# Performance work log

Hardware: AMD Instinct MI355X
Metric: run time of the kernel (lower is better)

Reference implementation:

```python
import jax, jax.numpy as jnp
import numpy as np

N_EXPERTS = 8
D_MODEL = 1024
D_FFN = 4096
BATCH, SEQ = 4, 1024


def setup_inputs() -> dict:
    key = jax.random.key(0)
    ks = jax.random.split(key, 12)
    T = BATCH * SEQ
    s_d = 1.0 / np.sqrt(D_MODEL)
    s_f = 1.0 / np.sqrt(D_FFN)
    return {
        "x": jax.random.normal(ks[0], (BATCH, SEQ, D_MODEL), jnp.float32),
        "noise": jax.random.normal(ks[1], (T, N_EXPERTS), jnp.float32),
        # router (torch Linear stored as [out,in]; we store pre-transposed [in,out])
        "Wg": jax.random.uniform(ks[2], (D_MODEL, N_EXPERTS), jnp.float32, -s_d, s_d),
        "bg": jax.random.uniform(ks[3], (N_EXPERTS,), jnp.float32, -s_d, s_d),
        "Wn": jax.random.uniform(ks[4], (D_MODEL, N_EXPERTS), jnp.float32, -s_d, s_d),
        "bn": jax.random.uniform(ks[5], (N_EXPERTS,), jnp.float32, -s_d, s_d),
        # stacked expert weights: fc1 [E, D, F], fc2 [E, F, D]
        "W1": jax.random.uniform(ks[6], (N_EXPERTS, D_MODEL, D_FFN), jnp.float32, -s_d, s_d),
        "b1": jax.random.uniform(ks[7], (N_EXPERTS, D_FFN), jnp.float32, -s_d, s_d),
        "W2": jax.random.uniform(ks[8], (N_EXPERTS, D_FFN, D_MODEL), jnp.float32, -s_f, s_f),
        "b2": jax.random.uniform(ks[9], (N_EXPERTS, D_MODEL), jnp.float32, -s_f, s_f),
        "top_k": 2,
    }


def reference(x, noise, Wg, bg, Wn, bn, W1, b1, W2, b2, top_k):
    B, S, D = x.shape
    xf = x.reshape(-1, D)                       # [T, D]
    T = xf.shape[0]
    # --- noisy top-k router ---
    logits = xf @ Wg + bg                       # [T, E]
    noise_logits = xf @ Wn + bn                 # [T, E]
    noisy = logits + noise * jax.nn.softplus(noise_logits)
    top_v, top_i = jax.lax.top_k(noisy, top_k)  # [T, k]
    sparse = jnp.full_like(noisy, -jnp.inf)
    sparse = sparse.at[jnp.arange(T)[:, None], top_i].set(top_v)
    gates = jax.nn.softmax(sparse, axis=-1)     # [T, E], zeros off top-k
    # --- experts (dense grouped GEMM; non-selected tokens zeroed by gates) ---
    h = jax.nn.relu(jnp.einsum('td,edf->etf', xf, W1) + b1[:, None, :])  # [E, T, F]
    eo = jnp.einsum('etf,efd->etd', h, W2) + b2[:, None, :]              # [E, T, D]
    out = jnp.einsum('etd,te->td', eo, gates)                            # [T, D]
    return out.reshape(B, S, D)
```

## Files before the change

kernel.cpp:

```cpp
#include <hip/hip_runtime.h>
#include <math.h>

#define T_TOK 4096
#define DM 1024
#define DF 4096
#define NE 8

#define BM 128
#define BN 128
#define BK 64

typedef __attribute__((ext_vector_type(8))) short bf16x8;
typedef __attribute__((ext_vector_type(4))) float f32x4;
typedef unsigned long long u64;

__device__ __forceinline__ unsigned short f2bf(float f) {
    union { float f; unsigned int u; } v; v.f = f;
    unsigned int r = v.u + 0x7FFFu + ((v.u >> 16) & 1u);
    return (unsigned short)(r >> 16);
}
__device__ __forceinline__ float bf2f(unsigned short u) {
    union { float f; unsigned int u; } v; v.u = ((unsigned int)u) << 16;
    return v.f;
}
__device__ __forceinline__ u64 pk4(float4 a) {
    return (u64)f2bf(a.x) | ((u64)f2bf(a.y) << 16) | ((u64)f2bf(a.z) << 32) | ((u64)f2bf(a.w) << 48);
}

__device__ __forceinline__ void glds16(const void* g, void* l) {
    __builtin_amdgcn_global_load_lds(
        (const __attribute__((address_space(1))) unsigned int*)g,
        (__attribute__((address_space(3))) unsigned int*)l, 16, 0, 0);
}

__global__ __launch_bounds__(256) void k_router(
    const float* __restrict__ x, const float* __restrict__ noise,
    const float* __restrict__ Wg, const float* __restrict__ bg,
    const float* __restrict__ Wn, const float* __restrict__ bn,
    int* __restrict__ counts, int* __restrict__ slots, float* __restrict__ gates,
    unsigned short* __restrict__ xb)
{
    const int lane = threadIdx.x & 63;
    const int wave = threadIdx.x >> 6;
    const int t = blockIdx.x * 4 + wave;
    const float* xr = x + (size_t)t * DM;

    float4 xv[4];
    #pragma unroll
    for (int j = 0; j < 4; ++j) xv[j] = *(const float4*)(xr + j * 256 + lane * 4);
    #pragma unroll
    for (int j = 0; j < 4; ++j)
        *(u64*)(xb + (size_t)t * DM + j * 256 + lane * 4) = pk4(xv[j]);

    float accg[8], accn[8];
    #pragma unroll
    for (int i = 0; i < 8; ++i) { accg[i] = 0.f; accn[i] = 0.f; }

    #pragma unroll
    for (int j = 0; j < 4; ++j) {
        const float xs[4] = {xv[j].x, xv[j].y, xv[j].z, xv[j].w};
        #pragma unroll
        for (int jj = 0; jj < 4; ++jj) {
            int d = j * 256 + lane * 4 + jj;
            float xvv = xs[jj];
            float4 g0 = *(const float4*)(Wg + d * 8);
            float4 g1 = *(const float4*)(Wg + d * 8 + 4);
            float4 n0 = *(const float4*)(Wn + d * 8);
            float4 n1 = *(const float4*)(Wn + d * 8 + 4);
            accg[0] += xvv * g0.x; accg[1] += xvv * g0.y; accg[2] += xvv * g0.z; accg[3] += xvv * g0.w;
            accg[4] += xvv * g1.x; accg[5] += xvv * g1.y; accg[6] += xvv * g1.z; accg[7] += xvv * g1.w;
            accn[0] += xvv * n0.x; accn[1] += xvv * n0.y; accn[2] += xvv * n0.z; accn[3] += xvv * n0.w;
            accn[4] += xvv * n1.x; accn[5] += xvv * n1.y; accn[6] += xvv * n1.z; accn[7] += xvv * n1.w;
        }
    }
    #pragma unroll
    for (int s = 1; s < 64; s <<= 1) {
        #pragma unroll
        for (int e = 0; e < 8; ++e) {
            accg[e] += __shfl_xor(accg[e], s, 64);
            accn[e] += __shfl_xor(accn[e], s, 64);
        }
    }
    if (lane == 0) {
        float nv[8];
        #pragma unroll
        for (int e = 0; e < 8; ++e) {
            float lg = accg[e] + bg[e];
            float nl = accn[e] + bn[e];
            float sp = (nl > 20.f) ? nl : log1pf(expf(nl));
            nv[e] = lg + noise[(size_t)t * NE + e] * sp;
        }
        int i0 = 0;
        #pragma unroll
        for (int e = 1; e < 8; ++e) if (nv[e] > nv[i0]) i0 = e;
        int i1 = -1;
        #pragma unroll
        for (int e = 0; e < 8; ++e) {
            if (e == i0) continue;
            if (i1 < 0 || nv[e] > nv[i1]) i1 = e;
        }
        float ex = expf(nv[i1] - nv[i0]);
        float g0 = 1.f / (1.f + ex);
        float g1 = ex / (1.f + ex);
        int p0 = atomicAdd(counts + i0, 1);
        slots[i0 * T_TOK + p0] = t * 2;     gates[i0 * T_TOK + p0] = g0;
        int p1 = atomicAdd(counts + i1, 1);
        slots[i1 * T_TOK + p1] = t * 2 + 1; gates[i1 * T_TOK + p1] = g1;
    }
}

__global__ __launch_bounds__(256) void k_tr(const float* __restrict__ in,
                                            unsigned short* __restrict__ out,
                                            int R, int C)
{
    __shared__ unsigned short t[64 * 68];
    const int e = blockIdx.z;
    const int C0 = blockIdx.x * 64, R0 = blockIdx.y * 64;
    const float* ip = in + ((size_t)e * R + R0) * C + C0;
    unsigned short* op = out + ((size_t)e * C + C0) * R + R0;
    const int tid = threadIdx.x;

    #pragma unroll
    for (int p = 0; p < 4; ++p) {
        int r = p * 16 + (tid >> 4), c4 = (tid & 15) * 4;
        float4 v = *(const float4*)(ip + (size_t)r * C + c4);
        t[(c4 + 0) * 68 + r] = f2bf(v.x);
        t[(c4 + 1) * 68 + r] = f2bf(v.y);
        t[(c4 + 2) * 68 + r] = f2bf(v.z);
        t[(c4 + 3) * 68 + r] = f2bf(v.w);
    }
    __syncthreads();
    #pragma unroll
    for (int p = 0; p < 4; ++p) {
        int c = p * 16 + (tid >> 4), r4 = (tid & 15) * 4;
        u64 v = *(const u64*)(t + c * 68 + r4);
        *(u64*)(op + (size_t)c * R + r4) = v;
    }
}

__global__ __launch_bounds__(256, 4) void k_fc1(
    const unsigned short* __restrict__ xb, const unsigned short* __restrict__ W1t,
    const float* __restrict__ b1, const int* __restrict__ counts,
    const int* __restrict__ slots, unsigned short* __restrict__ h)
{
    const int e = blockIdx.x;
    const int cnt = counts[e];
    const int mt = blockIdx.z;
    if (mt * BM >= cnt) return;
    const int nb = blockIdx.y * BN;

    int offE = 0;
    for (int i = 0; i < e; ++i) offE += counts[i];

    __shared__ unsigned short As[BM * BK];
    __shared__ unsigned short Bs[BN * BK];
    __shared__ int slot_s[BM];

    const int tid = threadIdx.x;
    if (tid < BM) {
        int gi = mt * BM + tid;
        slot_s[tid] = (gi < cnt) ? slots[e * T_TOK + gi] : -1;
    }
    __syncthreads();

    const int lane = tid & 63, wv = tid >> 6;
    const int srow = tid >> 3;
    const int g = (tid & 7) ^ (srow & 7);

    const unsigned short* agp[4];
    const unsigned short* bgp[4];
    const unsigned short* wbase = W1t + (size_t)e * DF * DM;
    #pragma unroll
    for (int cc = 0; cc < 4; ++cc) {
        int row = cc * 32 + srow;
        int s = slot_s[row];
        int tok = (s >= 0) ? (s >> 1) : 0;
        agp[cc] = xb + (size_t)tok * DM + g * 8;
        bgp[cc] = wbase + (size_t)(nb + row) * DM + g * 8;
    }
    unsigned short* al = As + wv * 512;
    unsigned short* bl = Bs + wv * 512;

    const int wm = (wv & 1) * 64, wn = (wv >> 1) * 64;
    const int ml = lane & 15, kg = lane >> 4;

    f32x4 acc[4][4];
    #pragma unroll
    for (int ni = 0; ni < 4; ++ni)
        #pragma unroll
        for (int mi = 0; mi < 4; ++mi) acc[ni][mi] = (f32x4){0.f, 0.f, 0.f, 0.f};

    for (int k0 = 0; k0 < DM; k0 += BK) {
        #pragma unroll
        for (int cc = 0; cc < 4; ++cc) glds16(agp[cc] + k0, al + cc * 2048);
        #pragma unroll
        for (int cc = 0; cc < 4; ++cc) glds16(bgp[cc] + k0, bl + cc * 2048);
        __syncthreads();
        #pragma unroll
        for (int ks = 0; ks < 2; ++ks) {
            const int rch = (((ks * 4 + kg) ^ (ml & 7)) << 3);
            bf16x8 af[4], bfr[4];
            #pragma unroll
            for (int mi = 0; mi < 4; ++mi)
                af[mi] = *(const bf16x8*)(As + (wm + mi * 16 + ml) * BK + rch);
            #pragma unroll
            for (int ni = 0; ni < 4; ++ni)
                bfr[ni] = *(const bf16x8*)(Bs + (wn + ni * 16 + ml) * BK + rch);
            #pragma unroll
            for (int ni = 0; ni < 4; ++ni)
                #pragma unroll
                for (int mi = 0; mi < 4; ++mi)
                    acc[ni][mi] = __builtin_amdgcn_mfma_f32_16x16x32_bf16(bfr[ni], af[mi], acc[ni][mi], 0, 0, 0);
        }
        __syncthreads();
    }

    #pragma unroll
    for (int mi = 0; mi < 4; ++mi) {
        int row = wm + mi * 16 + ml;
        int s = slot_s[row];
        if (s < 0) continue;
        unsigned short* hrow = h + (size_t)(offE + mt * BM + row) * DF + nb;
        #pragma unroll
        for (int ni = 0; ni < 4; ++ni) {
            int n0 = wn + ni * 16 + kg * 4;
            float4 bb = *(const float4*)(b1 + (size_t)e * DF + nb + n0);
            float v0 = fmaxf(acc[ni][mi][0] + bb.x, 0.f);
            float v1 = fmaxf(acc[ni][mi][1] + bb.y, 0.f);
            float v2 = fmaxf(acc[ni][mi][2] + bb.z, 0.f);
            float v3 = fmaxf(acc[ni][mi][3] + bb.w, 0.f);
            u64 p = (u64)f2bf(v0) | ((u64)f2bf(v1) << 16) | ((u64)f2bf(v2) << 32) | ((u64)f2bf(v3) << 48);
            *(u64*)(hrow + n0) = p;
        }
    }
}

__global__ __launch_bounds__(256, 4) void k_fc2(
    const unsigned short* __restrict__ h, const unsigned short* __restrict__ W2t,
    const float* __restrict__ b2, const int* __restrict__ counts,
    const int* __restrict__ slots, const float* __restrict__ gates,
    unsigned short* __restrict__ eo)
{
    const int e = blockIdx.x;
    const int cnt = counts[e];
    const int mt = blockIdx.z >> 1;
    const int kz = blockIdx.z & 1;
    if (mt * BM >= cnt) return;
    const int nb = blockIdx.y * BN;

    int offE = 0;
    for (int i = 0; i < e; ++i) offE += counts[i];

    __shared__ unsigned short As[BM * BK];
    __shared__ unsigned short Bs[BN * BK];
    __shared__ int slot_s[BM];
    __shared__ float gate_s[BM];

    const int tid = threadIdx.x;
    if (tid < BM) {
        int gi = mt * BM + tid;
        if (gi < cnt) {
            slot_s[tid] = slots[e * T_TOK + gi];
            gate_s[tid] = gates[e * T_TOK + gi];
        } else { slot_s[tid] = -1; gate_s[tid] = 0.f; }
    }
    __syncthreads();

    const int lane = tid & 63, wv = tid >> 6;
    const int srow = tid >> 3;
    const int g = (tid & 7) ^ (srow & 7);
    const int kbeg = kz * (DF / 2);

    const unsigned short* agp[4];
    const unsigned short* bgp[4];
    const unsigned short* wbase = W2t + (size_t)e * DM * DF;
    #pragma unroll
    for (int cc = 0; cc < 4; ++cc) {
        int row = cc * 32 + srow;
        int gi = mt * BM + row;
        int gpos = offE + ((gi < cnt) ? gi : 0);
        agp[cc] = h + (size_t)gpos * DF + kbeg + g * 8;
        bgp[cc] = wbase + (size_t)(nb + row) * DF + kbeg + g * 8;
    }
    unsigned short* al = As + wv * 512;
    unsigned short* bl = Bs + wv * 512;

    const int wm = (wv & 1) * 64, wn = (wv >> 1) * 64;
    const int ml = lane & 15, kg = lane >> 4;

    f32x4 acc[4][4];
    #pragma unroll
    for (int ni = 0; ni < 4; ++ni)
        #pragma unroll
        for (int mi = 0; mi < 4; ++mi) acc[ni][mi] = (f32x4){0.f, 0.f, 0.f, 0.f};

    for (int k0 = 0; k0 < DF / 2; k0 += BK) {
        #pragma unroll
        for (int cc = 0; cc < 4; ++cc) glds16(agp[cc] + k0, al + cc * 2048);
        #pragma unroll
        for (int cc = 0; cc < 4; ++cc) glds16(bgp[cc] + k0, bl + cc * 2048);
        __syncthreads();
        #pragma unroll
        for (int ks = 0; ks < 2; ++ks) {
            const int rch = (((ks * 4 + kg) ^ (ml & 7)) << 3);
            bf16x8 af[4], bfr[4];
            #pragma unroll
            for (int mi = 0; mi < 4; ++mi)
                af[mi] = *(const bf16x8*)(As + (wm + mi * 16 + ml) * BK + rch);
            #pragma unroll
            for (int ni = 0; ni < 4; ++ni)
                bfr[ni] = *(const bf16x8*)(Bs + (wn + ni * 16 + ml) * BK + rch);
            #pragma unroll
            for (int ni = 0; ni < 4; ++ni)
                #pragma unroll
                for (int mi = 0; mi < 4; ++mi)
                    acc[ni][mi] = __builtin_amdgcn_mfma_f32_16x16x32_bf16(bfr[ni], af[mi], acc[ni][mi], 0, 0, 0);
        }
        __syncthreads();
    }

    unsigned short* eob = eo + (size_t)kz * 2 * T_TOK * DM;
    #pragma unroll
    for (int mi = 0; mi < 4; ++mi) {
        int row = wm + mi * 16 + ml;
        int s = slot_s[row];
        if (s < 0) continue;
        float gg = gate_s[row];
        #pragma unroll
        for (int ni = 0; ni < 4; ++ni) {
            int n0 = wn + ni * 16 + kg * 4;
            float4 bb;
            if (kz == 0) bb = *(const float4*)(b2 + (size_t)e * DM + nb + n0);
            else         bb = make_float4(0.f, 0.f, 0.f, 0.f);
            float v0 = gg * (acc[ni][mi][0] + bb.x);
            float v1 = gg * (acc[ni][mi][1] + bb.y);
            float v2 = gg * (acc[ni][mi][2] + bb.z);
            float v3 = gg * (acc[ni][mi][3] + bb.w);
            u64 p = (u64)f2bf(v0) | ((u64)f2bf(v1) << 16) | ((u64)f2bf(v2) << 32) | ((u64)f2bf(v3) << 48);
            *(u64*)(eob + (size_t)s * DM + nb + n0) = p;
        }
    }
}

__global__ __launch_bounds__(256) void k_comb(const unsigned short* __restrict__ eo,
                                              float* __restrict__ out)
{
    int i = blockIdx.x * 256 + threadIdx.x;
    int t = i >> 8;
    int d4 = (i & 255) * 4;
    const unsigned short* p0 = eo + (size_t)(2 * t) * DM + d4;
    const unsigned short* p1 = p0 + DM;
    const unsigned short* q0 = p0 + (size_t)2 * T_TOK * DM;
    const unsigned short* q1 = q0 + DM;
    ushort4 a0 = *(const ushort4*)p0;
    ushort4 a1 = *(const ushort4*)p1;
    ushort4 b0 = *(const ushort4*)q0;
    ushort4 b1 = *(const ushort4*)q1;
    float4 r;
    r.x = bf2f(a0.x) + bf2f(a1.x) + bf2f(b0.x) + bf2f(b1.x);
    r.y = bf2f(a0.y) + bf2f(a1.y) + bf2f(b0.y) + bf2f(b1.y);
    r.z = bf2f(a0.z) + bf2f(a1.z) + bf2f(b0.z) + bf2f(b1.z);
    r.w = bf2f(a0.w) + bf2f(a1.w) + bf2f(b0.w) + bf2f(b1.w);
    ((float4*)out)[i] = r;
}

extern "C" void kernel_launch(void* const* d_in, const int* in_sizes, int n_in,
                              void* d_out, int out_size, void* d_ws, size_t ws_size,
                              hipStream_t stream) {
    const float* x     = (const float*)d_in[0];
    const float* noise = (const float*)d_in[1];
    const float* Wg    = (const float*)d_in[2];
    const float* bg    = (const float*)d_in[3];
    const float* Wn    = (const float*)d_in[4];
    const float* bn    = (const float*)d_in[5];
    const float* W1    = (const float*)d_in[6];
    const float* b1    = (const float*)d_in[7];
    const float* W2    = (const float*)d_in[8];
    const float* b2    = (const float*)d_in[9];
    float* out = (float*)d_out;

    char* ws = (char*)d_ws;
    int*   counts = (int*)ws;
    int*   slots  = (int*)(ws + 4096);
    float* gates  = (float*)(ws + 4096 + NE * T_TOK * 4);
    unsigned short* xb = (unsigned short*)(ws + 4096 + 2 * NE * T_TOK * 4);
    unsigned short* hh = xb + (size_t)T_TOK * DM;
    unsigned short* Wt = hh + (size_t)2 * T_TOK * DF;
    unsigned short* eo = Wt + (size_t)NE * DM * DF;

    hipMemsetAsync(counts, 0, 4096, stream);

    k_router<<<T_TOK / 4, 256, 0, stream>>>(x, noise, Wg, bg, Wn, bn, counts, slots, gates, xb);

    k_tr<<<dim3(DF / 64, DM / 64, NE), 256, 0, stream>>>(W1, Wt, DM, DF);
    k_fc1<<<dim3(NE, DF / BN, T_TOK / BM), 256, 0, stream>>>(xb, Wt, b1, counts, slots, hh);

    k_tr<<<dim3(DM / 64, DF / 64, NE), 256, 0, stream>>>(W2, Wt, DF, DM);
    k_fc2<<<dim3(NE, DM / BN, (T_TOK / BM) * 2), 256, 0, stream>>>(hh, Wt, b2, counts, slots, gates, eo);

    k_comb<<<T_TOK * DM / 1024, 256, 0, stream>>>(eo, out);
}
```

Measured before the change: 760.3 us.

## Switch expert GEMMs to 32x32 MFMA with double-buffered LDS and wider split-K

New measurement: 824.1 us. 1.08x slower.

```diff
diff --git a/kernel.cpp b/kernel.cpp
--- a/kernel.cpp
+++ b/kernel.cpp
@@ -8,10 +8,10 @@
 
 #define BM 128
 #define BN 128
-#define BK 64
+#define BK 32
 
 typedef __attribute__((ext_vector_type(8))) short bf16x8;
-typedef __attribute__((ext_vector_type(4))) float f32x4;
+typedef __attribute__((ext_vector_type(16))) float f32x16;
 typedef unsigned long long u64;
 
 __device__ __forceinline__ unsigned short f2bf(float f) {
@@ -138,7 +138,7 @@
     }
 }
 
-__global__ __launch_bounds__(256, 4) void k_fc1(
+__global__ __launch_bounds__(256, 5) void k_fc1(
     const unsigned short* __restrict__ xb, const unsigned short* __restrict__ W1t,
     const float* __restrict__ b1, const int* __restrict__ counts,
     const int* __restrict__ slots, unsigned short* __restrict__ h)
@@ -152,215 +152,209 @@
     int offE = 0;
     for (int i = 0; i < e; ++i) offE += counts[i];
 
-    __shared__ unsigned short As[BM * BK];
-    __shared__ unsigned short Bs[BN * BK];
-    __shared__ int slot_s[BM];
+    __shared__ unsigned short As[2][4096];
+    __shared__ unsigned short Bs[2][4096];
 
     const int tid = threadIdx.x;
-    if (tid < BM) {
-        int gi = mt * BM + tid;
-        slot_s[tid] = (gi < cnt) ? slots[e * T_TOK + gi] : -1;
-    }
-    __syncthreads();
-
     const int lane = tid & 63, wv = tid >> 6;
-    const int srow = tid >> 3;
-    const int g = (tid & 7) ^ (srow & 7);
-
-    const unsigned short* agp[4];
-    const unsigned short* bgp[4];
-    const unsigned short* wbase = W1t + (size_t)e * DF * DM;
-    #pragma unroll
-    for (int cc = 0; cc < 4; ++cc) {
-        int row = cc * 32 + srow;
-        int s = slot_s[row];
-        int tok = (s >= 0) ? (s >> 1) : 0;
-        agp[cc] = xb + (size_t)tok * DM + g * 8;
-        bgp[cc] = wbase + (size_t)(nb + row) * DM + g * 8;
-    }
-    unsigned short* al = As + wv * 512;
-    unsigned short* bl = Bs + wv * 512;
+
+    const int srow = tid & 127;
+    const int pl0 = tid >> 7;
+    int sgi = mt * BM + srow;
+    int sA = (sgi < cnt) ? slots[e * T_TOK + sgi] : -1;
+    int tok = (sA >= 0) ? (sA >> 1) : 0;
+    const unsigned short* aptr = xb + (size_t)tok * DM + pl0 * 8;
+    const unsigned short* bptr = W1t + (size_t)e * DF * DM + (size_t)(nb + srow) * DM + pl0 * 8;
+    unsigned short* alds = &As[0][tid * 8];
+    unsigned short* blds = &Bs[0][tid * 8];
 
     const int wm = (wv & 1) * 64, wn = (wv >> 1) * 64;
-    const int ml = lane & 15, kg = lane >> 4;
-
-    f32x4 acc[4][4];
-    #pragma unroll
-    for (int ni = 0; ni < 4; ++ni)
-        #pragma unroll
-        for (int mi = 0; mi < 4; ++mi) acc[ni][mi] = (f32x4){0.f, 0.f, 0.f, 0.f};
-
+    const int l31 = lane & 31, lh = lane >> 5;
+
+    f32x16 acc[2][2];
+    #pragma unroll
+    for (int ni = 0; ni < 2; ++ni)
+        #pragma unroll
+        for (int mi = 0; mi < 2; ++mi)
+            #pragma unroll
+            for (int r = 0; r < 16; ++r) acc[ni][mi][r] = 0.f;
+
+    glds16(aptr, alds);           glds16(aptr + 16, alds + 2048);
+    glds16(bptr, blds);           glds16(bptr + 16, blds + 2048);
+
+    int buf = 0;
     for (int k0 = 0; k0 < DM; k0 += BK) {
-        #pragma unroll
-        for (int cc = 0; cc < 4; ++cc) glds16(agp[cc] + k0, al + cc * 2048);
-        #pragma unroll
-        for (int cc = 0; cc < 4; ++cc) glds16(bgp[cc] + k0, bl + cc * 2048);
         __syncthreads();
+        if (k0 + BK < DM) {
+            int kn = k0 + BK;
+            unsigned short* an = &As[buf ^ 1][tid * 8];
+            unsigned short* bn2 = &Bs[buf ^ 1][tid * 8];
+            glds16(aptr + kn, an);           glds16(aptr + kn + 16, an + 2048);
+            glds16(bptr + kn, bn2);          glds16(bptr + kn + 16, bn2 + 2048);
+        }
         #pragma unroll
         for (int ks = 0; ks < 2; ++ks) {
-            const int rch = (((ks * 4 + kg) ^ (ml & 7)) << 3);
-            bf16x8 af[4], bfr[4];
-            #pragma unroll
-            for (int mi = 0; mi < 4; ++mi)
-                af[mi] = *(const bf16x8*)(As + (wm + mi * 16 + ml) * BK + rch);
-            #pragma unroll
-            for (int ni = 0; ni < 4; ++ni)
-                bfr[ni] = *(const bf16x8*)(Bs + (wn + ni * 16 + ml) * BK + rch);
-            #pragma unroll
-            for (int ni = 0; ni < 4; ++ni)
+            const int pbase = (ks * 2 + lh) * 1024;
+            bf16x8 af[2], bfr[2];
+            #pragma unroll
+            for (int mi = 0; mi < 2; ++mi)
+                af[mi] = *(const bf16x8*)(&As[buf][pbase + (wm + mi * 32 + l31) * 8]);
+            #pragma unroll
+            for (int ni = 0; ni < 2; ++ni)
+                bfr[ni] = *(const bf16x8*)(&Bs[buf][pbase + (wn + ni * 32 + l31) * 8]);
+            #pragma unroll
+            for (int ni = 0; ni < 2; ++ni)
                 #pragma unroll
-                for (int mi = 0; mi < 4; ++mi)
-                    acc[ni][mi] = __builtin_amdgcn_mfma_f32_16x16x32_bf16(bfr[ni], af[mi], acc[ni][mi], 0, 0, 0);
-        }
-        __syncthreads();
-    }
-
-    #pragma unroll
-    for (int mi = 0; mi < 4; ++mi) {
-        int row = wm + mi * 16 + ml;
-        int s = slot_s[row];
-        if (s < 0) continue;
-        unsigned short* hrow = h + (size_t)(offE + mt * BM + row) * DF + nb;
-        #pragma unroll
-        for (int ni = 0; ni < 4; ++ni) {
-            int n0 = wn + ni * 16 + kg * 4;
-            float4 bb = *(const float4*)(b1 + (size_t)e * DF + nb + n0);
-            float v0 = fmaxf(acc[ni][mi][0] + bb.x, 0.f);
-            float v1 = fmaxf(acc[ni][mi][1] + bb.y, 0.f);
-            float v2 = fmaxf(acc[ni][mi][2] + bb.z, 0.f);
-            float v3 = fmaxf(acc[ni][mi][3] + bb.w, 0.f);
-            u64 p = (u64)f2bf(v0) | ((u64)f2bf(v1) << 16) | ((u64)f2bf(v2) << 32) | ((u64)f2bf(v3) << 48);
-            *(u64*)(hrow + n0) = p;
-        }
-    }
-}
-
-__global__ __launch_bounds__(256, 4) void k_fc2(
+                for (int mi = 0; mi < 2; ++mi)
+                    acc[ni][mi] = __builtin_amdgcn_mfma_f32_32x32x16_bf16(bfr[ni], af[mi], acc[ni][mi], 0, 0, 0);
+        }
+        buf ^= 1;
+    }
+
+    #pragma unroll
+    for (int mi = 0; mi < 2; ++mi) {
+        int tcol = wm + mi * 32 + l31;
+        int gi = mt * BM + tcol;
+        if (gi >= cnt) continue;
+        unsigned short* hrow = h + (size_t)(offE + gi) * DF + nb;
+        #pragma unroll
+        for (int ni = 0; ni < 2; ++ni) {
+            #pragma unroll
+            for (int g = 0; g < 4; ++g) {
+                int n0 = wn + ni * 32 + 8 * g + 4 * lh;
+                float4 bb = *(const float4*)(b1 + (size_t)e * DF + nb + n0);
+                float v0 = fmaxf(acc[ni][mi][4 * g + 0] + bb.x, 0.f);
+                float v1 = fmaxf(acc[ni][mi][4 * g + 1] + bb.y, 0.f);
+                float v2 = fmaxf(acc[ni][mi][4 * g + 2] + bb.z, 0.f);
+                float v3 = fmaxf(acc[ni][mi][4 * g + 3] + bb.w, 0.f);
+                u64 p = (u64)f2bf(v0) | ((u64)f2bf(v1) << 16) | ((u64)f2bf(v2) << 32) | ((u64)f2bf(v3) << 48);
+                *(u64*)(hrow + n0) = p;
+            }
+        }
+    }
+}
+
+__global__ __launch_bounds__(256, 5) void k_fc2(
     const unsigned short* __restrict__ h, const unsigned short* __restrict__ W2t,
     const float* __restrict__ b2, const int* __restrict__ counts,
     const int* __restrict__ slots, const float* __restrict__ gates,
-    unsigned short* __restrict__ eo)
+    unsigned short* __restrict__ eo, int KZ, int klen)
 {
     const int e = blockIdx.x;
     const int cnt = counts[e];
-    const int mt = blockIdx.z >> 1;
-    const int kz = blockIdx.z & 1;
+    const int zz = blockIdx.z;
+    const int mt = zz / KZ;
+    const int kz = zz - mt * KZ;
     if (mt * BM >= cnt) return;
     const int nb = blockIdx.y * BN;
 
     int offE = 0;
     for (int i = 0; i < e; ++i) offE += counts[i];
 
-    __shared__ unsigned short As[BM * BK];
-    __shared__ unsigned short Bs[BN * BK];
-    __shared__ int slot_s[BM];
-    __shared__ float gate_s[BM];
+    __shared__ unsigned short As[2][4096];
+    __shared__ unsigned short Bs[2][4096];
 
     const int tid = threadIdx.x;
-    if (tid < BM) {
-        int gi = mt * BM + tid;
-        if (gi < cnt) {
-            slot_s[tid] = slots[e * T_TOK + gi];
-            gate_s[tid] = gates[e * T_TOK + gi];
-        } else { slot_s[tid] = -1; gate_s[tid] = 0.f; }
-    }
-    __syncthreads();
-
     const int lane = tid & 63, wv = tid >> 6;
-    const int srow = tid >> 3;
-    const int g = (tid & 7) ^ (srow & 7);
-    const int kbeg = kz * (DF / 2);
-
-    const unsigned short* agp[4];
-    const unsigned short* bgp[4];
-    const unsigned short* wbase = W2t + (size_t)e * DM * DF;
-    #pragma unroll
-    for (int cc = 0; cc < 4; ++cc) {
-        int row = cc * 32 + srow;
-        int gi = mt * BM + row;
-        int gpos = offE + ((gi < cnt) ? gi : 0);
-        agp[cc] = h + (size_t)gpos * DF + kbeg + g * 8;
-        bgp[cc] = wbase + (size_t)(nb + row) * DF + kbeg + g * 8;
-    }
-    unsigned short* al = As + wv * 512;
-    unsigned short* bl = Bs + wv * 512;
+
+    const int srow = tid & 127;
+    const int pl0 = tid >> 7;
+    int sgi = mt * BM + srow;
+    int gpos = offE + ((sgi < cnt) ? sgi : 0);
+    const int kbeg = kz * klen;
+    const unsigned short* aptr = h + (size_t)gpos * DF + kbeg + pl0 * 8;
+    const unsigned short* bptr = W2t + (size_t)e * DM * DF + (size_t)(nb + srow) * DF + kbeg + pl0 * 8;
+    unsigned short* alds = &As[0][tid * 8];
+    unsigned short* blds = &Bs[0][tid * 8];
 
     const int wm = (wv & 1) * 64, wn = (wv >> 1) * 64;
-    const int ml = lane & 15, kg = lane >> 4;
-
-    f32x4 acc[4][4];
-    #pragma unroll
-    for (int ni = 0; ni < 4; ++ni)
-        #pragma unroll
-        for (int mi = 0; mi < 4; ++mi) acc[ni][mi] = (f32x4){0.f, 0.f, 0.f, 0.f};
-
-    for (int k0 = 0; k0 < DF / 2; k0 += BK) {
-        #pragma unroll
-        for (int cc = 0; cc < 4; ++cc) glds16(agp[cc] + k0, al + cc * 2048);
-        #pragma unroll
-        for (int cc = 0; cc < 4; ++cc) glds16(bgp[cc] + k0, bl + cc * 2048);
+    const int l31 = lane & 31, lh = lane >> 5;
+
+    f32x16 acc[2][2];
+    #pragma unroll
+    for (int ni = 0; ni < 2; ++ni)
+        #pragma unroll
+        for (int mi = 0; mi < 2; ++mi)
+            #pragma unroll
+            for (int r = 0; r < 16; ++r) acc[ni][mi][r] = 0.f;
+
+    glds16(aptr, alds);           glds16(aptr + 16, alds + 2048);
+    glds16(bptr, blds);           glds16(bptr + 16, blds + 2048);
+
+    int buf = 0;
+    for (int k0 = 0; k0 < klen; k0 += BK) {
         __syncthreads();
+        if (k0 + BK < klen) {
+            int kn = k0 + BK;
+            unsigned short* an = &As[buf ^ 1][tid * 8];
+            unsigned short* bn2 = &Bs[buf ^ 1][tid * 8];
+            glds16(aptr + kn, an);           glds16(aptr + kn + 16, an + 2048);
+            glds16(bptr + kn, bn2);          glds16(bptr + kn + 16, bn2 + 2048);
+        }
         #pragma unroll
         for (int ks = 0; ks < 2; ++ks) {
-            const int rch = (((ks * 4 + kg) ^ (ml & 7)) << 3);
-            bf16x8 af[4], bfr[4];
-            #pragma unroll
-            for (int mi = 0; mi < 4; ++mi)
-                af[mi] = *(const bf16x8*)(As + (wm + mi * 16 + ml) * BK + rch);
-            #pragma unroll
-            for (int ni = 0; ni < 4; ++ni)
-                bfr[ni] = *(const bf16x8*)(Bs + (wn + ni * 16 + ml) * BK + rch);
-            #pragma unroll
-            for (int ni = 0; ni < 4; ++ni)
+            const int pbase = (ks * 2 + lh) * 1024;
+            bf16x8 af[2], bfr[2];
+            #pragma unroll
+            for (int mi = 0; mi < 2; ++mi)
+                af[mi] = *(const bf16x8*)(&As[buf][pbase + (wm + mi * 32 + l31) * 8]);
+            #pragma unroll
+            for (int ni = 0; ni < 2; ++ni)
+                bfr[ni] = *(const bf16x8*)(&Bs[buf][pbase + (wn + ni * 32 + l31) * 8]);
+            #pragma unroll
+            for (int ni = 0; ni < 2; ++ni)
                 #pragma unroll
-                for (int mi = 0; mi < 4; ++mi)
-                    acc[ni][mi] = __builtin_amdgcn_mfma_f32_16x16x32_bf16(bfr[ni], af[mi], acc[ni][mi], 0, 0, 0);
-        }
-        __syncthreads();
+                for (int mi = 0; mi < 2; ++mi)
+                    acc[ni][mi] = __builtin_amdgcn_mfma_f32_32x32x16_bf16(bfr[ni], af[mi], acc[ni][mi], 0, 0, 0);
+        }
+        buf ^= 1;
     }
 
     unsigned short* eob = eo + (size_t)kz * 2 * T_TOK * DM;
     #pragma unroll
-    for (int mi = 0; mi < 4; ++mi) {
-        int row = wm + mi * 16 + ml;
-        int s = slot_s[row];
-        if (s < 0) continue;
-        float gg = gate_s[row];
-        #pragma unroll
-        for (int ni = 0; ni < 4; ++ni) {
-            int n0 = wn + ni * 16 + kg * 4;
-            float4 bb;
-            if (kz == 0) bb = *(const float4*)(b2 + (size_t)e * DM + nb + n0);
-            else         bb = make_float4(0.f, 0.f, 0.f, 0.f);
-            float v0 = gg * (acc[ni][mi][0] + bb.x);
-            float v1 = gg * (acc[ni][mi][1] + bb.y);
-            float v2 = gg * (acc[ni][mi][2] + bb.z);
-            float v3 = gg * (acc[ni][mi][3] + bb.w);
-            u64 p = (u64)f2bf(v0) | ((u64)f2bf(v1) << 16) | ((u64)f2bf(v2) << 32) | ((u64)f2bf(v3) << 48);
-            *(u64*)(eob + (size_t)s * DM + nb + n0) = p;
+    for (int mi = 0; mi < 2; ++mi) {
+        int tcol = wm + mi * 32 + l31;
+        int gi = mt * BM + tcol;
+        if (gi >= cnt) continue;
+        int s = slots[e * T_TOK + gi];
+        float gg = gates[e * T_TOK + gi];
+        unsigned short* erow = eob + (size_t)s * DM + nb;
+        #pragma unroll
+        for (int ni = 0; ni < 2; ++ni) {
+            #pragma unroll
+            for (int g = 0; g < 4; ++g) {
+                int n0 = wn + ni * 32 + 8 * g + 4 * lh;
+                float4 bb;
+                if (kz == 0) bb = *(const float4*)(b2 + (size_t)e * DM + nb + n0);
+                else         bb = make_float4(0.f, 0.f, 0.f, 0.f);
+                float v0 = gg * (acc[ni][mi][4 * g + 0] + bb.x);
+                float v1 = gg * (acc[ni][mi][4 * g + 1] + bb.y);
+                float v2 = gg * (acc[ni][mi][4 * g + 2] + bb.z);
+                float v3 = gg * (acc[ni][mi][4 * g + 3] + bb.w);
+                u64 p = (u64)f2bf(v0) | ((u64)f2bf(v1) << 16) | ((u64)f2bf(v2) << 32) | ((u64)f2bf(v3) << 48);
+                *(u64*)(erow + n0) = p;
+            }
         }
     }
 }
 
 __global__ __launch_bounds__(256) void k_comb(const unsigned short* __restrict__ eo,
-                                              float* __restrict__ out)
+                                              float* __restrict__ out, int KZ)
 {
     int i = blockIdx.x * 256 + threadIdx.x;
     int t = i >> 8;
     int d4 = (i & 255) * 4;
-    const unsigned short* p0 = eo + (size_t)(2 * t) * DM + d4;
-    const unsigned short* p1 = p0 + DM;
-    const unsigned short* q0 = p0 + (size_t)2 * T_TOK * DM;
-    const unsigned short* q1 = q0 + DM;
-    ushort4 a0 = *(const ushort4*)p0;
-    ushort4 a1 = *(const ushort4*)p1;
-    ushort4 b0 = *(const ushort4*)q0;
-    ushort4 b1 = *(const ushort4*)q1;
-    float4 r;
-    r.x = bf2f(a0.x) + bf2f(a1.x) + bf2f(b0.x) + bf2f(b1.x);
-    r.y = bf2f(a0.y) + bf2f(a1.y) + bf2f(b0.y) + bf2f(b1.y);
-    r.z = bf2f(a0.z) + bf2f(a1.z) + bf2f(b0.z) + bf2f(b1.z);
-    r.w = bf2f(a0.w) + bf2f(a1.w) + bf2f(b0.w) + bf2f(b1.w);
+    float4 r = make_float4(0.f, 0.f, 0.f, 0.f);
+    const unsigned short* base = eo + (size_t)(2 * t) * DM + d4;
+    for (int kz = 0; kz < KZ; ++kz) {
+        const unsigned short* p0 = base + (size_t)kz * 2 * T_TOK * DM;
+        ushort4 a0 = *(const ushort4*)p0;
+        ushort4 a1 = *(const ushort4*)(p0 + DM);
+        r.x += bf2f(a0.x) + bf2f(a1.x);
+        r.y += bf2f(a0.y) + bf2f(a1.y);
+        r.z += bf2f(a0.z) + bf2f(a1.z);
+        r.w += bf2f(a0.w) + bf2f(a1.w);
+    }
     ((float4*)out)[i] = r;
 }
 
@@ -388,6 +382,11 @@
     unsigned short* Wt = hh + (size_t)2 * T_TOK * DF;
     unsigned short* eo = Wt + (size_t)NE * DM * DF;
 
+    size_t base_bytes = (size_t)((char*)eo - ws);
+    size_t slice = (size_t)2 * T_TOK * DM * 2;
+    int KZ = (ws_size >= base_bytes + 4 * slice) ? 4 : 2;
+    int klen = DF / KZ;
+
     hipMemsetAsync(counts, 0, 4096, stream);
 
     k_router<<<T_TOK / 4, 256, 0, stream>>>(x, noise, Wg, bg, Wn, bn, counts, slots, gates, xb);
@@ -396,7 +395,7 @@
     k_fc1<<<dim3(NE, DF / BN, T_TOK / BM), 256, 0, stream>>>(xb, Wt, b1, counts, slots, hh);
 
     k_tr<<<dim3(DM / 64, DF / 64, NE), 256, 0, stream>>>(W2, Wt, DF, DM);
-    k_fc2<<<dim3(NE, DM / BN, (T_TOK / BM) * 2), 256, 0, stream>>>(hh, Wt, b2, counts, slots, gates, eo);
-
-    k_comb<<<T_TOK * DM / 1024, 256, 0, stream>>>(eo, out);
-}
+    k_fc2<<<dim3(NE, DM / BN, (T_TOK / BM) * KZ), 256, 0, stream>>>(hh, Wt, b2, counts, slots, gates, eo, KZ, klen);
+
+    k_comb<<<T_TOK * DM / 1024, 256, 0, stream>>>(eo, out, KZ);
+}
```
